# Performance work log

Hardware: AMD Instinct MI355X
Metric: run time of the kernel (lower is better)

Reference implementation:

```python
import jax, jax.numpy as jnp
import numpy as np

N_USER = 100000
N_ITEM = 100000
N_EDGE = 1000000
IN_DIM = 256
HID = 128
OUT = 16
LEAKY_SLOPE = 0.01  # torch F.leaky_relu default


def _seg_mean(msg, dst, num_segments):
    # segment mean with zero in-degree -> 0 (DGL mean semantics)
    s = jax.ops.segment_sum(msg, dst, num_segments=num_segments)
    c = jax.ops.segment_sum(jnp.ones((dst.shape[0], 1), msg.dtype), dst, num_segments=num_segments)
    return jnp.where(c > 0, s / jnp.maximum(c, 1.0), 0.0)


def setup_inputs() -> dict:
    key = jax.random.key(0)
    ks = jax.random.split(key, 24)
    def lin(k, fan_in, fan_out):
        # torch nn.Linear init: U(-1/sqrt(fan_in), 1/sqrt(fan_in)) for W and b
        bound = 1.0 / np.sqrt(fan_in)
        kw, kb = jax.random.split(k)
        W = jax.random.uniform(kw, (fan_in, fan_out), jnp.float32, -bound, bound)
        b = jax.random.uniform(kb, (fan_out,), jnp.float32, -bound, bound)
        return W, b
    inp = {}
    inp['feat_user'] = jax.random.normal(ks[0], (N_USER, IN_DIM), jnp.float32)
    inp['feat_item'] = jax.random.normal(ks[1], (N_ITEM, IN_DIM), jnp.float32)
    inp['src_clicks'] = jax.random.randint(ks[2], (N_EDGE,), 0, N_USER, jnp.int32)
    inp['dst_clicks'] = jax.random.randint(ks[3], (N_EDGE,), 0, N_ITEM, jnp.int32)
    inp['src_cb'] = jax.random.randint(ks[4], (N_EDGE,), 0, N_ITEM, jnp.int32)
    inp['dst_cb'] = jax.random.randint(ks[5], (N_EDGE,), 0, N_USER, jnp.int32)
    inp['Win_user'], inp['bin_user'] = lin(ks[6], IN_DIM, HID)
    inp['Win_item'], inp['bin_item'] = lin(ks[7], IN_DIM, HID)
    inp['W0_clicks'], inp['b0_clicks'] = lin(ks[8], HID, HID)
    inp['W0_cb'], inp['b0_cb'] = lin(ks[9], HID, HID)
    inp['W1_clicks'], inp['b1_clicks'] = lin(ks[10], HID, HID)
    inp['W1_cb'], inp['b1_cb'] = lin(ks[11], HID, HID)
    inp['Wout'], inp['bout'] = lin(ks[12], HID, OUT)
    return inp


def reference(feat_user, feat_item, src_clicks, dst_clicks, src_cb, dst_cb,
              Win_user, bin_user, Win_item, bin_item,
              W0_clicks, b0_clicks, W0_cb, b0_cb,
              W1_clicks, b1_clicks, W1_cb, b1_cb,
              Wout, bout):
    # input projections per node type
    x_u = feat_user @ Win_user + bin_user   # [N_USER, HID]
    x_i = feat_item @ Win_item + bin_item   # [N_ITEM, HID]

    def layer(x_u, x_i, Wc, bc, Wcb, bcb):
        # per-relation Linear on source nodes, then copy_u gather + mean scatter
        wh_u = x_u @ Wc + bc                 # user -> clicks -> item
        wh_i = x_i @ Wcb + bcb               # item -> clicked_by -> user
        h_i = _seg_mean(wh_u[src_clicks], dst_clicks, N_ITEM)
        h_u = _seg_mean(wh_i[src_cb], dst_cb, N_USER)
        return h_u, h_i

    h_u, h_i = layer(x_u, x_i, W0_clicks, b0_clicks, W0_cb, b0_cb)
    h_u = jax.nn.leaky_relu(h_u, LEAKY_SLOPE)
    h_i = jax.nn.leaky_relu(h_i, LEAKY_SLOPE)
    h_u, h_i = layer(h_u, h_i, W1_clicks, b1_clicks, W1_cb, b1_cb)

    # final projection on target_node = 'user'
    return h_u @ Wout + bout
```

## Files before the change

kernel.cpp:

```cpp
#include <hip/hip_runtime.h>
#include <hip/hip_bf16.h>
#include <cstddef>
#include <cstdint>

#define N_USER 100000
#define N_ITEM 100000
#define N_EDGE 1000000
#define IN_DIM 256
#define HID 128
#define OUT_DIM 16
#define LEAKY_SLOPE 0.01f
#define SRC_MASK 0x07FFFFFFu

#define NC 98
#define CAPB 12288
#define TILE 4096

typedef __attribute__((ext_vector_type(8))) short bf16x8;
typedef __attribute__((ext_vector_type(4))) float f32x4;

static __device__ __forceinline__ unsigned short f2bf(float f) {
  unsigned int u = __float_as_uint(f);
  u = (u + 0x7FFFu + ((u >> 16) & 1u)) >> 16;
  return (unsigned short)u;
}

static __device__ __forceinline__ void split8(const float4 x, const float4 y,
                                              bf16x8& hi, bf16x8& lo) {
  const float f[8] = {x.x, x.y, x.z, x.w, y.x, y.y, y.z, y.w};
#pragma unroll
  for (int j = 0; j < 8; ++j) {
    const unsigned u = __float_as_uint(f[j]);
    hi[j] = (short)(u >> 16);
    const float lf = f[j] - __uint_as_float(u & 0xffff0000u);
    lo[j] = (short)(__float_as_uint(lf) >> 16);
  }
}

__global__ __launch_bounds__(256)
void part_coarse(const int* __restrict__ srcA, const int* __restrict__ dstA,
                 const int* __restrict__ srcB, const int* __restrict__ dstB,
                 int* __restrict__ gcur, uint32_t* __restrict__ tmp, int n) {
  __shared__ uint32_t srec[TILE];
  __shared__ unsigned char sbkt[TILE];
  __shared__ int hist[NC], lofs[NC], gbase[NC], lcur[NC];
  const int y = blockIdx.y, t = threadIdx.x;
  const int* __restrict__ src = y ? srcB : srcA;
  const int* __restrict__ dst = y ? dstB : dstA;
  const int e0 = blockIdx.x * TILE;
  const int ne = min(TILE, n - e0);

  for (int i = t; i < NC; i += 256) hist[i] = 0;
  __syncthreads();

  uint32_t rec[16];
  int bk[16];
#pragma unroll
  for (int q = 0; q < 16; ++q) {
    const int i = t + q * 256;
    if (i < ne) {
      const int d = dst[e0 + i];
      rec[q] = (uint32_t)src[e0 + i] | ((uint32_t)(d & 1023) << 17);
      bk[q] = d >> 10;
      atomicAdd(&hist[bk[q]], 1);
    } else {
      bk[q] = -1;
    }
  }
  __syncthreads();

  if (t == 0) {
    int run = 0;
#pragma unroll 1
    for (int i = 0; i < NC; ++i) { lofs[i] = run; run += hist[i]; }
  }
  __syncthreads();
  if (t < NC) {
    lcur[t] = 0;
    gbase[t] = atomicAdd(&gcur[y * NC + t], hist[t]);
  }
  __syncthreads();

#pragma unroll
  for (int q = 0; q < 16; ++q) {
    if (bk[q] >= 0) {
      const int p = lofs[bk[q]] + atomicAdd(&lcur[bk[q]], 1);
      srec[p] = rec[q];
      sbkt[p] = (unsigned char)bk[q];
    }
  }
  __syncthreads();

  uint32_t* __restrict__ outp = tmp + (size_t)y * NC * CAPB;
  for (int i = t; i < ne; i += 256) {
    const int b = sbkt[i];
    outp[(size_t)b * CAPB + gbase[b] + (i - lofs[b])] = srec[i];
  }
}

__global__ __launch_bounds__(256)
void part_fine(const uint32_t* __restrict__ tmp, const int* __restrict__ gcur,
               uint32_t* __restrict__ ebuf, int* __restrict__ pos,
               int* __restrict__ cnt) {
  __shared__ int dcnt[1024];
  __shared__ int sh[256];
  const int y = blockIdx.y, b = blockIdx.x, t = threadIdx.x;
  const int ne = gcur[y * NC + b];
  const uint32_t* __restrict__ in = tmp + ((size_t)y * NC + b) * CAPB;

  for (int i = t; i < 1024; i += 256) dcnt[i] = 0;
  __syncthreads();
  for (int i = t; i < ne; i += 256) atomicAdd(&dcnt[in[i] >> 17], 1);
  __syncthreads();

  const int bi = t * 4;
  const int v0 = dcnt[bi], v1 = dcnt[bi + 1], v2 = dcnt[bi + 2], v3 = dcnt[bi + 3];
  const int tsum = v0 + v1 + v2 + v3;
  sh[t] = tsum;
  __syncthreads();
#pragma unroll
  for (int d = 1; d < 256; d <<= 1) {
    const int x = (t >= d) ? sh[t - d] : 0;
    __syncthreads();
    sh[t] += x;
    __syncthreads();
  }
  const int p0 = sh[t] - tsum;
  const int p1 = p0 + v0, p2 = p1 + v1, p3 = p2 + v2;
  dcnt[bi] = p0; dcnt[bi + 1] = p1; dcnt[bi + 2] = p2; dcnt[bi + 3] = p3;

  const int drow0 = (b << 10) + bi;
  const int prel = b * CAPB;
  int* __restrict__ cw = cnt + (size_t)y * N_USER;
  int* __restrict__ pw = pos + (size_t)y * N_USER;
  if (drow0 + 0 < N_USER) { cw[drow0 + 0] = v0; pw[drow0 + 0] = prel + p0; }
  if (drow0 + 1 < N_USER) { cw[drow0 + 1] = v1; pw[drow0 + 1] = prel + p1; }
  if (drow0 + 2 < N_USER) { cw[drow0 + 2] = v2; pw[drow0 + 2] = prel + p2; }
  if (drow0 + 3 < N_USER) { cw[drow0 + 3] = v3; pw[drow0 + 3] = prel + p3; }
  __syncthreads();

  uint32_t* __restrict__ outp = ebuf + ((size_t)y * NC + b) * CAPB;
  for (int i = t; i < ne; i += 256) {
    const uint32_t r = in[i];
    const int p = atomicAdd(&dcnt[r >> 17], 1);
    outp[p] = r & 0x1FFFFu;
  }
}

__global__ __launch_bounds__(256)
void make_wfuse0(const float* __restrict__ Win, const float* __restrict__ bin,
                 const float* __restrict__ W0, const float* __restrict__ b0,
                 unsigned short* __restrict__ Bswz, float* __restrict__ bf0) {
  const int t = threadIdx.x;
  const int r = blockIdx.x * 2 + (t >> 7);
  const int n = t & 127;
  const float* wr = Win + (size_t)r * HID;
  float s = 0.f;
#pragma unroll 8
  for (int m = 0; m < HID; ++m) s += wr[m] * W0[(size_t)m * HID + n];
  const unsigned u = __float_as_uint(s);
  const unsigned short hi = (unsigned short)(u >> 16);
  const float lf = s - __uint_as_float(u & 0xffff0000u);
  const unsigned short lo = (unsigned short)(__float_as_uint(lf) >> 16);
  const int kt = r >> 5, lh = (r >> 3) & 3, j = r & 7;
  const int nf = n >> 4, lane = lh * 16 + (n & 15);
  Bswz[(size_t)(kt * 16 + nf * 2) * 512 + lane * 8 + j] = hi;
  Bswz[(size_t)(kt * 16 + nf * 2 + 1) * 512 + lane * 8 + j] = lo;
  if (blockIdx.x == 0 && t < HID) {
    float s2 = b0[t];
    for (int m = 0; m < HID; ++m) s2 += bin[m] * W0[(size_t)m * HID + t];
    bf0[t] = s2;
  }
}

__global__ __launch_bounds__(256, 2)
void gemm_feat_mfma(const float* __restrict__ A,
                    const unsigned short* __restrict__ Bswz,
                    const float* __restrict__ bias,
                    unsigned short* __restrict__ Wh, int M) {
  __shared__ unsigned short Bs[2][16384];
  const int t = threadIdx.x;
  const int w = t >> 6, lane = t & 63;
  const int rowW = blockIdx.x * 128 + w * 32;
  const int lr = lane & 15;
  const int lk = (lane >> 4) << 3;

  int r0 = rowW + lr;      if (r0 >= M) r0 = M - 1;
  int r1 = rowW + 16 + lr; if (r1 >= M) r1 = M - 1;
  const float* pa0 = A + (size_t)r0 * IN_DIM + lk;
  const float* pa1 = A + (size_t)r1 * IN_DIM + lk;

  float bv[8];
#pragma unroll
  for (int nf = 0; nf < 8; ++nf) bv[nf] = bias[nf * 16 + lr];

  f32x4 acc[2][8];
#pragma unroll
  for (int rf = 0; rf < 2; ++rf)
#pragma unroll
    for (int nf = 0; nf < 8; ++nf)
#pragma unroll
      for (int q = 0; q < 4; ++q) acc[rf][nf][q] = 0.f;

  float4 af[2][2][2][2];

#define STAGE_B(c, buf)                                                        \
  {                                                                            \
    _Pragma("unroll")                                                          \
    for (int i = 0; i < 8; ++i)                                                \
      __builtin_amdgcn_global_load_lds(                                        \
          (const __attribute__((address_space(1))) unsigned int*)              \
              ((const char*)Bswz + (c) * 32768 + i * 4096 + t * 16),           \
          (__attribute__((address_space(3))) unsigned int*)                    \
              &Bs[buf][i * 2048 + w * 512],                                    \
          16, 0, 0);                                                           \
  }

#define LOAD_A(c, buf)                                                         \
  {                                                                            \
    _Pragma("unroll")                                                          \
    for (int ktl = 0; ktl < 2; ++ktl) {                                        \
      af[buf][0][ktl][0] = *(const float4*)(pa0 + (c) * 64 + ktl * 32);        \
      af[buf][0][ktl][1] = *(const float4*)(pa0 + (c) * 64 + ktl * 32 + 4);    \
      af[buf][1][ktl][0] = *(const float4*)(pa1 + (c) * 64 + ktl * 32);        \
      af[buf][1][ktl][1] = *(const float4*)(pa1 + (c) * 64 + ktl * 32 + 4);    \
    }                                                                          \
  }

  STAGE_B(0, 0)
  LOAD_A(0, 0)
  __syncthreads();

#pragma unroll
  for (int c = 0; c < 4; ++c) {
    const int cb = c & 1;
    if (c < 3) {
      STAGE_B(c + 1, cb ^ 1)
      LOAD_A(c + 1, cb ^ 1)
    }
    bf16x8 ah[2][2], al[2][2];
#pragma unroll
    for (int rf = 0; rf < 2; ++rf)
#pragma unroll
      for (int ktl = 0; ktl < 2; ++ktl)
        split8(af[cb][rf][ktl][0], af[cb][rf][ktl][1], ah[rf][ktl], al[rf][ktl]);
#pragma unroll
    for (int ktl = 0; ktl < 2; ++ktl) {
#pragma unroll
      for (int nf = 0; nf < 8; ++nf) {
        const bf16x8 bh =
            *(const bf16x8*)&Bs[cb][(ktl * 16 + nf * 2) * 512 + lane * 8];
        const bf16x8 bl =
            *(const bf16x8*)&Bs[cb][(ktl * 16 + nf * 2 + 1) * 512 + lane * 8];
#pragma unroll
        for (int rf = 0; rf < 2; ++rf) {
          acc[rf][nf] = __builtin_amdgcn_mfma_f32_16x16x32_bf16(
              ah[rf][ktl], bh, acc[rf][nf], 0, 0, 0);
          acc[rf][nf] = __builtin_amdgcn_mfma_f32_16x16x32_bf16(
              ah[rf][ktl], bl, acc[rf][nf], 0, 0, 0);
          acc[rf][nf] = __builtin_amdgcn_mfma_f32_16x16x32_bf16(
              al[rf][ktl], bh, acc[rf][nf], 0, 0, 0);
        }
      }
    }
    __syncthreads();
  }
#undef STAGE_B
#undef LOAD_A

#pragma unroll
  for (int rf = 0; rf < 2; ++rf) {
#pragma unroll
    for (int i = 0; i < 4; ++i) {
      const int row = rowW + rf * 16 + ((lane >> 4) << 2) + i;
      if (row < M) {
        unsigned short* op = Wh + (size_t)row * HID + lr;
#pragma unroll
        for (int nf = 0; nf < 8; ++nf) op[nf * 16] = f2bf(acc[rf][nf][i] + bv[nf]);
      }
    }
  }
}

__global__ __launch_bounds__(256)
void make_wfuse(const float* __restrict__ W1, const float* __restrict__ b1,
                const float* __restrict__ Wout, const float* __restrict__ bout,
                float* __restrict__ Wf, float* __restrict__ bf) {
  __shared__ float Ws[HID * OUT_DIM];
  const int t = threadIdx.x;
  {
    const float4* s0 = (const float4*)Wout;
    float4* dp = (float4*)Ws;
    dp[t]       = s0[t];
    dp[t + 256] = s0[t + 256];
  }
  __syncthreads();
  const int k  = t >> 1;
  const int j0 = (t & 1) * 8;
  const float* w1row = W1 + (size_t)k * HID;
  float acc[8] = {0.f, 0.f, 0.f, 0.f, 0.f, 0.f, 0.f, 0.f};
  for (int m = 0; m < HID; ++m) {
    const float a = w1row[m];
    const float* wr = &Ws[m * OUT_DIM + j0];
#pragma unroll
    for (int q = 0; q < 8; ++q) acc[q] += a * wr[q];
  }
#pragma unroll
  for (int q = 0; q < 8; ++q) Wf[(size_t)k * OUT_DIM + j0 + q] = acc[q];
  if (t < OUT_DIM) {
    float s = bout[t];
    for (int m = 0; m < HID; ++m) s += b1[m] * Ws[m * OUT_DIM + t];
    bf[t] = s;
  }
}

static __device__ __forceinline__ void acc_bf8(float* a, uint4 u) {
  a[0] += __uint_as_float(u.x << 16);
  a[1] += __uint_as_float(u.x & 0xffff0000u);
  a[2] += __uint_as_float(u.y << 16);
  a[3] += __uint_as_float(u.y & 0xffff0000u);
  a[4] += __uint_as_float(u.z << 16);
  a[5] += __uint_as_float(u.z & 0xffff0000u);
  a[6] += __uint_as_float(u.w << 16);
  a[7] += __uint_as_float(u.w & 0xffff0000u);
}

__global__ __launch_bounds__(256)
void gather_mean_bf16(const unsigned short* __restrict__ bh,
                      const int* __restrict__ pos, const int* __restrict__ cnt,
                      const uint32_t* __restrict__ ebuf, float* __restrict__ out) {
  const int row = blockIdx.x * 16 + (threadIdx.x >> 4);
  const int c = threadIdx.x & 15;
  const int beg = pos[row];
  const int cn  = cnt[row];
  float acc[8] = {0.f, 0.f, 0.f, 0.f, 0.f, 0.f, 0.f, 0.f};
  int i = 0;
  for (; i + 4 <= cn; i += 4) {
    const int s0 = (int)(ebuf[beg + i]     & SRC_MASK);
    const int s1 = (int)(ebuf[beg + i + 1] & SRC_MASK);
    const int s2 = (int)(ebuf[beg + i + 2] & SRC_MASK);
    const int s3 = (int)(ebuf[beg + i + 3] & SRC_MASK);
    const uint4 v0 = *((const uint4*)(bh + (size_t)s0 * HID) + c);
    const uint4 v1 = *((const uint4*)(bh + (size_t)s1 * HID) + c);
    const uint4 v2 = *((const uint4*)(bh + (size_t)s2 * HID) + c);
    const uint4 v3 = *((const uint4*)(bh + (size_t)s3 * HID) + c);
    acc_bf8(acc, v0); acc_bf8(acc, v1); acc_bf8(acc, v2); acc_bf8(acc, v3);
  }
  for (; i < cn; ++i) {
    const int s = (int)(ebuf[beg + i] & SRC_MASK);
    const uint4 v = *((const uint4*)(bh + (size_t)s * HID) + c);
    acc_bf8(acc, v);
  }
  const float inv = cn > 0 ? 1.0f / (float)cn : 0.0f;
  float4 o0, o1;
  float r[8];
#pragma unroll
  for (int q = 0; q < 8; ++q) {
    float v = acc[q] * inv;
    r[q] = v > 0.f ? v : LEAKY_SLOPE * v;
  }
  o0 = make_float4(r[0], r[1], r[2], r[3]);
  o1 = make_float4(r[4], r[5], r[6], r[7]);
  float* op = out + (size_t)row * HID + c * 8;
  *(float4*)op = o0;
  *(float4*)(op + 4) = o1;
}

__global__ __launch_bounds__(256)
void gemm_z16(const float* __restrict__ H, const float* __restrict__ Wf,
              float* __restrict__ z, int M) {
  __shared__ float Ws[HID * OUT_DIM];
  __shared__ float Hs[16 * HID];
  const int t = threadIdx.x;
  const int row0 = blockIdx.x * 16;
  {
    const float4* s0 = (const float4*)Wf;
    float4* dp = (float4*)Ws;
    dp[t]       = s0[t];
    dp[t + 256] = s0[t + 256];
    const float4* s1 = (const float4*)(H + (size_t)row0 * HID);
    float4* hp = (float4*)Hs;
    hp[t]       = s1[t];
    hp[t + 256] = s1[t + 256];
  }
  __syncthreads();
  const int r = t >> 4, c = t & 15;
  float s = 0.f;
  const float* h = &Hs[r * HID];
#pragma unroll 8
  for (int k = 0; k < HID; ++k) s += h[k] * Ws[k * OUT_DIM + c];
  z[(size_t)(row0 + r) * OUT_DIM + c] = s;
}

__global__ __launch_bounds__(256)
void gather_mean16(const float* __restrict__ z, const int* __restrict__ pos,
                   const int* __restrict__ cnt, const uint32_t* __restrict__ ebuf,
                   const float* __restrict__ bfuse, const float* __restrict__ bout,
                   float* __restrict__ out) {
  const int row = blockIdx.x * 16 + (threadIdx.x >> 4);
  const int c = threadIdx.x & 15;
  const int beg = pos[row];
  const int cn  = cnt[row];
  float acc = 0.f;
  int i = 0;
  for (; i + 4 <= cn; i += 4) {
    const int s0 = (int)(ebuf[beg + i]     & SRC_MASK);
    const int s1 = (int)(ebuf[beg + i + 1] & SRC_MASK);
    const int s2 = (int)(ebuf[beg + i + 2] & SRC_MASK);
    const int s3 = (int)(ebuf[beg + i + 3] & SRC_MASK);
    const float v0 = z[(size_t)s0 * OUT_DIM + c];
    const float v1 = z[(size_t)s1 * OUT_DIM + c];
    const float v2 = z[(size_t)s2 * OUT_DIM + c];
    const float v3 = z[(size_t)s3 * OUT_DIM + c];
    acc += v0 + v1 + v2 + v3;
  }
  for (; i < cn; ++i) {
    const int s = (int)(ebuf[beg + i] & SRC_MASK);
    acc += z[(size_t)s * OUT_DIM + c];
  }
  float o;
  if (cn > 0) o = acc * (1.0f / (float)cn) + bfuse[c];
  else        o = bout[c];
  out[(size_t)row * OUT_DIM + c] = o;
}

extern "C" void kernel_launch(void* const* d_in, const int* in_sizes, int n_in,
                              void* d_out, int out_size, void* d_ws, size_t ws_size,
                              hipStream_t stream) {
  const float* feat_user  = (const float*)d_in[0];
  const int*   src_clicks = (const int*)d_in[2];
  const int*   dst_clicks = (const int*)d_in[3];
  const int*   src_cb     = (const int*)d_in[4];
  const int*   dst_cb     = (const int*)d_in[5];
  const float* Win_user   = (const float*)d_in[6];
  const float* bin_user   = (const float*)d_in[7];
  const float* W0_clicks  = (const float*)d_in[10];
  const float* b0_clicks  = (const float*)d_in[11];
  const float* W1_cb      = (const float*)d_in[16];
  const float* b1_cb      = (const float*)d_in[17];
  const float* Wout       = (const float*)d_in[18];
  const float* bout       = (const float*)d_in[19];
  float* out = (float*)d_out;

  const size_t SZ  = (size_t)N_USER * HID * sizeof(float);
  const size_t SZH = (size_t)N_USER * HID * sizeof(unsigned short);
  const size_t SZZ = (size_t)N_USER * OUT_DIM * sizeof(float);
  const size_t SZE = (size_t)2 * NC * CAPB * sizeof(uint32_t);
  char* ws = (char*)d_ws;
  float* buf0          = (float*)ws;
  uint32_t* tmp        = (uint32_t*)ws;
  unsigned short* bh   = (unsigned short*)(ws + SZ);
  float* z0            = (float*)(ws + SZ + SZH);
  unsigned short* Bswz = (unsigned short*)z0;
  float* bf0v          = (float*)((char*)z0 + 131072);
  float* Wf            = (float*)(ws + SZ + SZH + SZZ);
  float* bf            = Wf + HID * OUT_DIM;
  int* cnt  = (int*)(bf + OUT_DIM);
  int* pos  = cnt + 2 * N_USER;
  int* gcur = pos + 2 * N_USER;
  uint32_t* ebuf = (uint32_t*)(gcur + 2 * NC + 12);

  const int G16 = N_USER / 16;
  const int GM  = (N_USER + 127) / 128;
  const int GP  = (N_EDGE + TILE - 1) / TILE;

  hipMemsetAsync(gcur, 0, (size_t)2 * NC * sizeof(int), stream);
  part_coarse<<<dim3(GP, 2), 256, 0, stream>>>(src_clicks, dst_clicks,
                                               src_cb, dst_cb, gcur, tmp, N_EDGE);
  part_fine<<<dim3(NC, 2), 256, 0, stream>>>(tmp, gcur, ebuf, pos, cnt);

  make_wfuse<<<1, 256, 0, stream>>>(W1_cb, b1_cb, Wout, bout, Wf, bf);
  make_wfuse0<<<128, 256, 0, stream>>>(Win_user, bin_user, W0_clicks, b0_clicks,
                                       Bswz, bf0v);

  gemm_feat_mfma<<<GM, 256, 0, stream>>>(feat_user, Bswz, bf0v, bh, N_USER);
  gather_mean_bf16<<<G16, 256, 0, stream>>>(bh, pos, cnt, ebuf, buf0);
  gemm_z16<<<G16, 256, 0, stream>>>(buf0, Wf, z0, N_ITEM);
  gather_mean16<<<G16, 256, 0, stream>>>(z0, pos + N_USER, cnt + N_USER,
                                         ebuf + (size_t)NC * CAPB, bf, bout, out);
}
```

Before: 408.2 us.

## Fuse item gather-mean with z projection and use wave-per-row persistent gathers

Merges the bf16 gather-mean over clicks edges with the 128->16 fused projection, so each row's hidden vector is reduced in registers and multiplied by Wf instead of being written as a 51 MB fp32 buffer and re-read by a separate GEMM kernel. Both gather kernels now assign one 64-lane wave per destination row, split edges across four 16-lane groups, combine them with shuffles, and loop over rows in a fixed 2048-block grid. This removes one launch and the intermediate traffic. The cost is extra shuffle reductions per row and only 4-wide edge parallelism per wave, which may hurt latency hiding on rows with few edges.

```diff
diff --git a/kernel.cpp b/kernel.cpp
--- a/kernel.cpp
+++ b/kernel.cpp
@@ -326,102 +326,77 @@
 }
 
 __global__ __launch_bounds__(256)
-void gather_mean_bf16(const unsigned short* __restrict__ bh,
-                      const int* __restrict__ pos, const int* __restrict__ cnt,
-                      const uint32_t* __restrict__ ebuf, float* __restrict__ out) {
-  const int row = blockIdx.x * 16 + (threadIdx.x >> 4);
-  const int c = threadIdx.x & 15;
-  const int beg = pos[row];
-  const int cn  = cnt[row];
-  float acc[8] = {0.f, 0.f, 0.f, 0.f, 0.f, 0.f, 0.f, 0.f};
-  int i = 0;
-  for (; i + 4 <= cn; i += 4) {
-    const int s0 = (int)(ebuf[beg + i]     & SRC_MASK);
-    const int s1 = (int)(ebuf[beg + i + 1] & SRC_MASK);
-    const int s2 = (int)(ebuf[beg + i + 2] & SRC_MASK);
-    const int s3 = (int)(ebuf[beg + i + 3] & SRC_MASK);
-    const uint4 v0 = *((const uint4*)(bh + (size_t)s0 * HID) + c);
-    const uint4 v1 = *((const uint4*)(bh + (size_t)s1 * HID) + c);
-    const uint4 v2 = *((const uint4*)(bh + (size_t)s2 * HID) + c);
-    const uint4 v3 = *((const uint4*)(bh + (size_t)s3 * HID) + c);
-    acc_bf8(acc, v0); acc_bf8(acc, v1); acc_bf8(acc, v2); acc_bf8(acc, v3);
-  }
-  for (; i < cn; ++i) {
-    const int s = (int)(ebuf[beg + i] & SRC_MASK);
-    const uint4 v = *((const uint4*)(bh + (size_t)s * HID) + c);
-    acc_bf8(acc, v);
-  }
-  const float inv = cn > 0 ? 1.0f / (float)cn : 0.0f;
-  float4 o0, o1;
-  float r[8];
-#pragma unroll
-  for (int q = 0; q < 8; ++q) {
-    float v = acc[q] * inv;
-    r[q] = v > 0.f ? v : LEAKY_SLOPE * v;
-  }
-  o0 = make_float4(r[0], r[1], r[2], r[3]);
-  o1 = make_float4(r[4], r[5], r[6], r[7]);
-  float* op = out + (size_t)row * HID + c * 8;
-  *(float4*)op = o0;
-  *(float4*)(op + 4) = o1;
-}
-
-__global__ __launch_bounds__(256)
-void gemm_z16(const float* __restrict__ H, const float* __restrict__ Wf,
-              float* __restrict__ z, int M) {
-  __shared__ float Ws[HID * OUT_DIM];
-  __shared__ float Hs[16 * HID];
-  const int t = threadIdx.x;
-  const int row0 = blockIdx.x * 16;
-  {
-    const float4* s0 = (const float4*)Wf;
-    float4* dp = (float4*)Ws;
-    dp[t]       = s0[t];
-    dp[t + 256] = s0[t + 256];
-    const float4* s1 = (const float4*)(H + (size_t)row0 * HID);
-    float4* hp = (float4*)Hs;
-    hp[t]       = s1[t];
-    hp[t + 256] = s1[t + 256];
-  }
-  __syncthreads();
-  const int r = t >> 4, c = t & 15;
-  float s = 0.f;
-  const float* h = &Hs[r * HID];
-#pragma unroll 8
-  for (int k = 0; k < HID; ++k) s += h[k] * Ws[k * OUT_DIM + c];
-  z[(size_t)(row0 + r) * OUT_DIM + c] = s;
-}
-
-__global__ __launch_bounds__(256)
-void gather_mean16(const float* __restrict__ z, const int* __restrict__ pos,
-                   const int* __restrict__ cnt, const uint32_t* __restrict__ ebuf,
-                   const float* __restrict__ bfuse, const float* __restrict__ bout,
-                   float* __restrict__ out) {
-  const int row = blockIdx.x * 16 + (threadIdx.x >> 4);
-  const int c = threadIdx.x & 15;
-  const int beg = pos[row];
-  const int cn  = cnt[row];
-  float acc = 0.f;
-  int i = 0;
-  for (; i + 4 <= cn; i += 4) {
-    const int s0 = (int)(ebuf[beg + i]     & SRC_MASK);
-    const int s1 = (int)(ebuf[beg + i + 1] & SRC_MASK);
-    const int s2 = (int)(ebuf[beg + i + 2] & SRC_MASK);
-    const int s3 = (int)(ebuf[beg + i + 3] & SRC_MASK);
-    const float v0 = z[(size_t)s0 * OUT_DIM + c];
-    const float v1 = z[(size_t)s1 * OUT_DIM + c];
-    const float v2 = z[(size_t)s2 * OUT_DIM + c];
-    const float v3 = z[(size_t)s3 * OUT_DIM + c];
-    acc += v0 + v1 + v2 + v3;
-  }
-  for (; i < cn; ++i) {
-    const int s = (int)(ebuf[beg + i] & SRC_MASK);
-    acc += z[(size_t)s * OUT_DIM + c];
-  }
-  float o;
-  if (cn > 0) o = acc * (1.0f / (float)cn) + bfuse[c];
-  else        o = bout[c];
-  out[(size_t)row * OUT_DIM + c] = o;
+void gather_z_fused(const unsigned short* __restrict__ bh,
+                    const int* __restrict__ pos, const int* __restrict__ cnt,
+                    const uint32_t* __restrict__ ebuf,
+                    const float* __restrict__ Wf, float* __restrict__ z) {
+  const int lane = threadIdx.x & 63;
+  const int g = lane >> 4, c = lane & 15;
+  const int wid = (blockIdx.x * 256 + threadIdx.x) >> 6;
+  const int nw = gridDim.x * 4;
+  float4 wfv[8];
+#pragma unroll
+  for (int j = 0; j < 8; ++j)
+    wfv[j] = *(const float4*)&Wf[(c * 8 + j) * OUT_DIM + g * 4];
+
+  for (int row = wid; row < N_ITEM; row += nw) {
+    const int beg = pos[row];
+    const int cn  = cnt[row];
+    float acc[8] = {0.f, 0.f, 0.f, 0.f, 0.f, 0.f, 0.f, 0.f};
+    for (int i = g; i < cn; i += 4) {
+      const int s = (int)(ebuf[beg + i] & SRC_MASK);
+      const uint4 v = *((const uint4*)(bh + (size_t)s * HID) + c);
+      acc_bf8(acc, v);
+    }
+#pragma unroll
+    for (int j = 0; j < 8; ++j) {
+      acc[j] += __shfl_xor(acc[j], 16);
+      acc[j] += __shfl_xor(acc[j], 32);
+    }
+    const float inv = cn > 0 ? 1.0f / (float)cn : 0.0f;
+    float zx = 0.f, zy = 0.f, zz = 0.f, zw = 0.f;
+#pragma unroll
+    for (int j = 0; j < 8; ++j) {
+      float h = acc[j] * inv;
+      h = h > 0.f ? h : LEAKY_SLOPE * h;
+      zx += h * wfv[j].x; zy += h * wfv[j].y;
+      zz += h * wfv[j].z; zw += h * wfv[j].w;
+    }
+#pragma unroll
+    for (int m = 1; m < 16; m <<= 1) {
+      zx += __shfl_xor(zx, m);
+      zy += __shfl_xor(zy, m);
+      zz += __shfl_xor(zz, m);
+      zw += __shfl_xor(zw, m);
+    }
+    if (c < 4) {
+      const float zv = (c == 0) ? zx : (c == 1) ? zy : (c == 2) ? zz : zw;
+      z[(size_t)row * OUT_DIM + g * 4 + c] = zv;
+    }
+  }
+}
+
+__global__ __launch_bounds__(256)
+void gather_mean16_w(const float* __restrict__ z, const int* __restrict__ pos,
+                     const int* __restrict__ cnt, const uint32_t* __restrict__ ebuf,
+                     const float* __restrict__ bfuse, const float* __restrict__ bout,
+                     float* __restrict__ out) {
+  const int lane = threadIdx.x & 63;
+  const int g = lane >> 4, c = lane & 15;
+  const int wid = (blockIdx.x * 256 + threadIdx.x) >> 6;
+  const int nw = gridDim.x * 4;
+  const float bfv = bfuse[c], bov = bout[c];
+  for (int row = wid; row < N_USER; row += nw) {
+    const int beg = pos[row];
+    const int cn  = cnt[row];
+    float acc = 0.f;
+    for (int i = g; i < cn; i += 4)
+      acc += z[(size_t)(ebuf[beg + i] & SRC_MASK) * OUT_DIM + c];
+    acc += __shfl_xor(acc, 16);
+    acc += __shfl_xor(acc, 32);
+    if (g == 0)
+      out[(size_t)row * OUT_DIM + c] = cn > 0 ? acc / (float)cn + bfv : bov;
+  }
 }
 
 extern "C" void kernel_launch(void* const* d_in, const int* in_sizes, int n_in,
@@ -445,9 +420,7 @@
   const size_t SZ  = (size_t)N_USER * HID * sizeof(float);
   const size_t SZH = (size_t)N_USER * HID * sizeof(unsigned short);
   const size_t SZZ = (size_t)N_USER * OUT_DIM * sizeof(float);
-  const size_t SZE = (size_t)2 * NC * CAPB * sizeof(uint32_t);
   char* ws = (char*)d_ws;
-  float* buf0          = (float*)ws;
   uint32_t* tmp        = (uint32_t*)ws;
   unsigned short* bh   = (unsigned short*)(ws + SZ);
   float* z0            = (float*)(ws + SZ + SZH);
@@ -460,7 +433,6 @@
   int* gcur = pos + 2 * N_USER;
   uint32_t* ebuf = (uint32_t*)(gcur + 2 * NC + 12);
 
-  const int G16 = N_USER / 16;
   const int GM  = (N_USER + 127) / 128;
   const int GP  = (N_EDGE + TILE - 1) / TILE;
 
@@ -474,8 +446,7 @@
                                        Bswz, bf0v);
 
   gemm_feat_mfma<<<GM, 256, 0, stream>>>(feat_user, Bswz, bf0v, bh, N_USER);
-  gather_mean_bf16<<<G16, 256, 0, stream>>>(bh, pos, cnt, ebuf, buf0);
-  gemm_z16<<<G16, 256, 0, stream>>>(buf0, Wf, z0, N_ITEM);
-  gather_mean16<<<G16, 256, 0, stream>>>(z0, pos + N_USER, cnt + N_USER,
-                                         ebuf + (size_t)NC * CAPB, bf, bout, out);
-}
+  gather_z_fused<<<2048, 256, 0, stream>>>(bh, pos, cnt, ebuf, Wf, z0);
+  gather_mean16_w<<<2048, 256, 0, stream>>>(z0, pos + N_USER, cnt + N_USER,
+                                            ebuf + (size_t)NC * CAPB, bf, bout, out);
+}
```

Result: slower. 434.3 us (+6.4%).
